# Kernel tuning notes

Measured on AMD Instinct MI355X. Metric: run time of the kernel, lower is better.

Reference implementation:

```python
import jax, jax.numpy as jnp
import numpy as np

N_NODES = 100000

def setup_inputs() -> dict:
    key = jax.random.key(0)
    k1, k2, k3, k4 = jax.random.split(key, 4)
    feat = jax.random.normal(k1, (N_NODES, 128), dtype=jnp.float32)
    weight = jax.random.normal(k2, (128, 64), dtype=jnp.float32) * 0.05
    src = jax.random.randint(k3, (600000,), 0, N_NODES, dtype=jnp.int64)
    dst = jax.random.randint(k4, (600000,), 0, N_NODES, dtype=jnp.int64)
    return {"feat": feat, "weight": weight, "src": src, "dst": dst}

def reference(feat, weight, src, dst):
    n = feat.shape[0]
    ones = jnp.ones(src.shape[0], dtype=jnp.float32)
    # out-degree of source nodes (edges leave src), in-degree of dst nodes
    out_deg = jnp.clip(jax.ops.segment_sum(ones, src, num_segments=n), 1.0)
    in_deg = jnp.clip(jax.ops.segment_sum(ones, dst, num_segments=n), 1.0)
    norm_src = (out_deg ** -0.5)[:, None]   # [N,1]
    norm_dst = (in_deg ** -0.5)[:, None]    # [N,1]
    # in_feats (128) > out_feats (64): project first, then aggregate
    h = jnp.matmul(feat, weight) * norm_src              # [N, 64]
    msgs = h[src]                                        # [E, 64] gather
    rst = jax.ops.segment_sum(msgs, dst, num_segments=n)  # [N, 64] scatter-sum
    rst = rst * norm_dst
    return rst
```

## Files before the change

### kernel.cpp

```cpp
#include <hip/hip_runtime.h>
#include <hip/hip_fp16.h>

#define IN_F 128
#define OUT_F 64
#define NB    256
#define BSH   9
#define CAP   3840
#define CHUNK 2048
#define KPF  136
#define KPW  144

using short8  = __attribute__((ext_vector_type(8))) short;
using float4v = __attribute__((ext_vector_type(4))) float;

static __device__ inline unsigned short f2bf(float x) {
    union { float f; unsigned u; } v; v.f = x;
    unsigned r = (v.u + 0x7fffu + ((v.u >> 16) & 1u)) >> 16;
    return (unsigned short)r;
}

__global__ __launch_bounds__(256) void bin_gemm_kernel(
    const int* __restrict__ src, const int* __restrict__ dst,
    int* __restrict__ gcur_d, int* __restrict__ gcur_s,
    unsigned* __restrict__ bkt_d, unsigned short* __restrict__ bkt_s,
    int E, int nbin,
    const float* __restrict__ feat, const float* __restrict__ W,
    __half* __restrict__ h, int n)
{
    __shared__ union {
        struct { int hd[NB]; int hs[NB]; int based[NB]; int bases[NB]; } bin;
        struct { unsigned short Fh[128 * KPF]; unsigned short Wt[64 * KPW]; } gm;
    } smem;

    const int tid = threadIdx.x;
    const int b   = blockIdx.x;
    const int G   = gridDim.x;
    const int f   = (int)(((long)b       * nbin) / G);
    const int c   = (int)(((long)(b + 1) * nbin) / G);
    const bool is_bin = (c > f);

    if (is_bin) {
        const int e0 = f * CHUNK;

        smem.bin.hd[tid] = 0; smem.bin.hs[tid] = 0;
        __syncthreads();

        int sv[8], dv[8];
        #pragma unroll
        for (int j = 0; j < 8; ++j) {
            int i = e0 + j * 256 + tid;
            if (i < E) { sv[j] = src[i]; dv[j] = dst[i]; }
            else       { sv[j] = -1;     dv[j] = -1; }
        }
        #pragma unroll
        for (int j = 0; j < 8; ++j) {
            if (dv[j] >= 0) {
                atomicAdd(&smem.bin.hd[dv[j] >> BSH], 1);
                atomicAdd(&smem.bin.hs[sv[j] >> BSH], 1);
            }
        }
        __syncthreads();

        int cd = smem.bin.hd[tid], cs = smem.bin.hs[tid];
        smem.bin.based[tid] = cd ? atomicAdd(&gcur_d[tid], cd) : 0;
        smem.bin.bases[tid] = cs ? atomicAdd(&gcur_s[tid], cs) : 0;
        smem.bin.hd[tid] = 0; smem.bin.hs[tid] = 0;
        __syncthreads();

        #pragma unroll
        for (int j = 0; j < 8; ++j) {
            if (dv[j] >= 0) {
                int bd = dv[j] >> BSH;
                int pd = atomicAdd(&smem.bin.hd[bd], 1) + smem.bin.based[bd];
                if (pd < CAP)
                    bkt_d[(size_t)bd * CAP + pd] =
                        (unsigned)sv[j] | ((unsigned)(dv[j] & 511) << 17);
                int bs = sv[j] >> BSH;
                int ps = atomicAdd(&smem.bin.hs[bs], 1) + smem.bin.bases[bs];
                if (ps < CAP) bkt_s[(size_t)bs * CAP + ps] = (unsigned short)(sv[j] & 511);
            }
        }
        return;
    }

    unsigned short* Fh = smem.gm.Fh;
    unsigned short* Wt = smem.gm.Wt;
    const int row0 = (b - f) * 128;

    {
        const float4* W4 = (const float4*)W;
        #pragma unroll
        for (int it = 0; it < 8; ++it) {
            int i4 = it * 256 + tid;
            int k  = i4 >> 4;
            int c4 = (i4 & 15) * 4;
            float4 wv = W4[i4];
            Wt[(c4 + 0) * KPW + k] = f2bf(wv.x);
            Wt[(c4 + 1) * KPW + k] = f2bf(wv.y);
            Wt[(c4 + 2) * KPW + k] = f2bf(wv.z);
            Wt[(c4 + 3) * KPW + k] = f2bf(wv.w);
        }
    }
    {
        const float4* F4 = (const float4*)feat;
        #pragma unroll
        for (int it = 0; it < 16; ++it) {
            int i4 = it * 256 + tid;
            int r  = i4 >> 5;
            int c4 = (i4 & 31) * 4;
            int gr = row0 + r; if (gr >= n) gr = n - 1;
            float4 v = F4[(long)gr * 32 + (i4 & 31)];
            ushort4 u;
            u.x = f2bf(v.x); u.y = f2bf(v.y); u.z = f2bf(v.z); u.w = f2bf(v.w);
            *(ushort4*)&Fh[r * KPF + c4] = u;
        }
    }
    __syncthreads();

    const int w  = tid >> 6;
    const int l  = tid & 63;
    const int ml = l & 15;
    const int q  = l >> 4;

    float4v acc[2][4];
    #pragma unroll
    for (int rt = 0; rt < 2; ++rt)
        #pragma unroll
        for (int ct = 0; ct < 4; ++ct)
            acc[rt][ct] = (float4v){0.f, 0.f, 0.f, 0.f};

    #pragma unroll
    for (int ks = 0; ks < 4; ++ks) {
        const int ko = ks * 32 + q * 8;
        short8 a0 = *(const short8*)&Fh[(w * 32 +  0 + ml) * KPF + ko];
        short8 a1 = *(const short8*)&Fh[(w * 32 + 16 + ml) * KPF + ko];
        short8 b0 = *(const short8*)&Wt[( 0 + ml) * KPW + ko];
        short8 b1 = *(const short8*)&Wt[(16 + ml) * KPW + ko];
        short8 b2 = *(const short8*)&Wt[(32 + ml) * KPW + ko];
        short8 b3 = *(const short8*)&Wt[(48 + ml) * KPW + ko];
        acc[0][0] = __builtin_amdgcn_mfma_f32_16x16x32_bf16(a0, b0, acc[0][0], 0, 0, 0);
        acc[0][1] = __builtin_amdgcn_mfma_f32_16x16x32_bf16(a0, b1, acc[0][1], 0, 0, 0);
        acc[0][2] = __builtin_amdgcn_mfma_f32_16x16x32_bf16(a0, b2, acc[0][2], 0, 0, 0);
        acc[0][3] = __builtin_amdgcn_mfma_f32_16x16x32_bf16(a0, b3, acc[0][3], 0, 0, 0);
        acc[1][0] = __builtin_amdgcn_mfma_f32_16x16x32_bf16(a1, b0, acc[1][0], 0, 0, 0);
        acc[1][1] = __builtin_amdgcn_mfma_f32_16x16x32_bf16(a1, b1, acc[1][1], 0, 0, 0);
        acc[1][2] = __builtin_amdgcn_mfma_f32_16x16x32_bf16(a1, b2, acc[1][2], 0, 0, 0);
        acc[1][3] = __builtin_amdgcn_mfma_f32_16x16x32_bf16(a1, b3, acc[1][3], 0, 0, 0);
    }

    #pragma unroll
    for (int rt = 0; rt < 2; ++rt) {
        #pragma unroll
        for (int reg = 0; reg < 4; ++reg) {
            int row = row0 + w * 32 + rt * 16 + q * 4 + reg;
            if (row < n) {
                #pragma unroll
                for (int ct = 0; ct < 4; ++ct)
                    h[(long)row * OUT_F + ct * 16 + ml] = __float2half(acc[rt][ct][reg]);
            }
        }
    }
}

__global__ __launch_bounds__(256) void csr_kernel(
    const unsigned* __restrict__ bkt_d, const unsigned short* __restrict__ bkt_s,
    const int* __restrict__ gcur_d, const int* __restrict__ gcur_s,
    int2* __restrict__ off_deg, int* __restrict__ ebuf, float* __restrict__ nsrc, int n)
{
    __shared__ int hist[512], curs[512], hist_s[512];
    __shared__ int wsum[4];
    const int b = blockIdx.x, tid = threadIdx.x;
    const int cnt   = min(gcur_d[b], CAP);
    const int cnt_s = min(gcur_s[b], CAP);

    hist[tid] = 0; hist[tid + 256] = 0;
    hist_s[tid] = 0; hist_s[tid + 256] = 0;
    __syncthreads();

    const unsigned* bp = bkt_d + (size_t)b * CAP;
    for (int i = tid; i < cnt; i += 256)
        atomicAdd(&hist[bp[i] >> 17], 1);
    for (int i = tid; i < cnt_s; i += 256)
        atomicAdd(&hist_s[bkt_s[(size_t)b * CAP + i]], 1);
    __syncthreads();

    int a0 = hist[2 * tid], a1 = hist[2 * tid + 1];
    int psum = a0 + a1;
    const int lane = tid & 63, w = tid >> 6;
    int x = psum;
    #pragma unroll
    for (int off = 1; off < 64; off <<= 1) {
        int y = __shfl_up(x, off);
        if (lane >= off) x += y;
    }
    if (lane == 63) wsum[w] = x;
    __syncthreads();
    int wbase = 0;
    for (int i = 0; i < w; ++i) wbase += wsum[i];
    int excl = x + wbase - psum;
    curs[2 * tid]     = excl;
    curs[2 * tid + 1] = excl + a0;
    off_deg[b * 512 + 2 * tid]     = make_int2(b * CAP + excl,      a0);
    off_deg[b * 512 + 2 * tid + 1] = make_int2(b * CAP + excl + a0, a1);
    __syncthreads();

    for (int i = tid; i < cnt; i += 256) {
        unsigned e = bp[i];
        int p = atomicAdd(&curs[e >> 17], 1);
        if (p < CAP) ebuf[b * CAP + p] = (int)(e & 0x1FFFFu);
    }

    int node = b * 512 + tid;
    if (node < n) nsrc[node] = rsqrtf(fmaxf((float)hist_s[tid], 1.0f));
    node += 256;
    if (node < n) nsrc[node] = rsqrtf(fmaxf((float)hist_s[tid + 256], 1.0f));
}

__global__ __launch_bounds__(256) void gather_kernel(
    const int* __restrict__ ebuf, const int2* __restrict__ off_deg,
    const float* __restrict__ nsrc,
    const __half* __restrict__ h, float* __restrict__ out, int n)
{
    const int lane = threadIdx.x & 63;
    const int wv   = threadIdx.x >> 6;
    const int o    = lane >> 3;
    const int t    = lane & 7;
    const int d    = blockIdx.x * 32 + wv * 8 + o;
    if (d >= n) return;

    int2 od = off_deg[d];
    const int beg = od.x, m = od.y, end = beg + m;

    float a0 = 0.f, a1 = 0.f, a2 = 0.f, a3 = 0.f;
    float a4 = 0.f, a5 = 0.f, a6 = 0.f, a7 = 0.f;

    int j = beg;
    for (; j + 1 < end; j += 2) {
        int sA = ebuf[j];
        int sB = ebuf[j + 1];
        float nsA = nsrc[sA];
        float nsB = nsrc[sB];
        union { uint4 u; __half2 h2[4]; } PA, PB;
        PA.u = *(const uint4*)&h[(long)sA * OUT_F + 8 * t];
        PB.u = *(const uint4*)&h[(long)sB * OUT_F + 8 * t];
        float2 fA0 = __half22float2(PA.h2[0]);
        float2 fA1 = __half22float2(PA.h2[1]);
        float2 fA2 = __half22float2(PA.h2[2]);
        float2 fA3 = __half22float2(PA.h2[3]);
        a0 = fmaf(fA0.x, nsA, a0); a1 = fmaf(fA0.y, nsA, a1);
        a2 = fmaf(fA1.x, nsA, a2); a3 = fmaf(fA1.y, nsA, a3);
        a4 = fmaf(fA2.x, nsA, a4); a5 = fmaf(fA2.y, nsA, a5);
        a6 = fmaf(fA3.x, nsA, a6); a7 = fmaf(fA3.y, nsA, a7);
        float2 fB0 = __half22float2(PB.h2[0]);
        float2 fB1 = __half22float2(PB.h2[1]);
        float2 fB2 = __half22float2(PB.h2[2]);
        float2 fB3 = __half22float2(PB.h2[3]);
        a0 = fmaf(fB0.x, nsB, a0); a1 = fmaf(fB0.y, nsB, a1);
        a2 = fmaf(fB1.x, nsB, a2); a3 = fmaf(fB1.y, nsB, a3);
        a4 = fmaf(fB2.x, nsB, a4); a5 = fmaf(fB2.y, nsB, a5);
        a6 = fmaf(fB3.x, nsB, a6); a7 = fmaf(fB3.y, nsB, a7);
    }
    if (j < end) {
        int s = ebuf[j];
        float ns = nsrc[s];
        union { uint4 u; __half2 h2[4]; } P;
        P.u = *(const uint4*)&h[(long)s * OUT_F + 8 * t];
        float2 f0 = __half22float2(P.h2[0]);
        float2 f1 = __half22float2(P.h2[1]);
        float2 f2 = __half22float2(P.h2[2]);
        float2 f3 = __half22float2(P.h2[3]);
        a0 = fmaf(f0.x, ns, a0); a1 = fmaf(f0.y, ns, a1);
        a2 = fmaf(f1.x, ns, a2); a3 = fmaf(f1.y, ns, a3);
        a4 = fmaf(f2.x, ns, a4); a5 = fmaf(f2.y, ns, a5);
        a6 = fmaf(f3.x, ns, a6); a7 = fmaf(f3.y, ns, a7);
    }

    float nd = rsqrtf(fmaxf((float)m, 1.0f));
    float4 v0 = make_float4(a0 * nd, a1 * nd, a2 * nd, a3 * nd);
    float4 v1 = make_float4(a4 * nd, a5 * nd, a6 * nd, a7 * nd);
    float* op = &out[(long)d * OUT_F + 8 * t];
    *(float4*)op       = v0;
    *(float4*)(op + 4) = v1;
}

extern "C" void kernel_launch(void* const* d_in, const int* in_sizes, int n_in,
                              void* d_out, int out_size, void* d_ws, size_t ws_size,
                              hipStream_t stream) {
    const float* feat = (const float*)d_in[0];
    const float* W    = (const float*)d_in[1];
    const int*   src  = (const int*)d_in[2];
    const int*   dst  = (const int*)d_in[3];
    float* out = (float*)d_out;

    const int n = in_sizes[0] / IN_F;
    const int E = in_sizes[2];

    char* wsb = (char*)d_ws;
    int* gcur_d = (int*)wsb;
    int* gcur_s = gcur_d + NB;
    float* nsrc = (float*)(gcur_s + NB);
    size_t pos = (((size_t)(2 * NB + n)) * 4 + 15) & ~(size_t)15;
    int2* off_deg = (int2*)(wsb + pos);
    pos = (pos + (size_t)NB * 512 * 8 + 15) & ~(size_t)15;
    int* ebuf = (int*)(wsb + pos);
    pos = (pos + (size_t)NB * CAP * 4 + 15) & ~(size_t)15;
    unsigned* bkt_d = (unsigned*)(wsb + pos);
    pos = (pos + (size_t)NB * CAP * 4 + 15) & ~(size_t)15;
    unsigned short* bkt_s = (unsigned short*)(wsb + pos);
    pos = (pos + (size_t)NB * CAP * 2 + 15) & ~(size_t)15;
    __half* h = (__half*)(wsb + pos);

    hipMemsetAsync(gcur_d, 0, 2 * NB * sizeof(int), stream);

    const int nbin  = (E + CHUNK - 1) / CHUNK;
    const int ngemm = (n + 127) / 128;

    bin_gemm_kernel<<<nbin + ngemm, 256, 0, stream>>>(src, dst, gcur_d, gcur_s,
                                                      bkt_d, bkt_s, E, nbin,
                                                      feat, W, h, n);
    csr_kernel<<<NB, 256, 0, stream>>>(bkt_d, bkt_s, gcur_d, gcur_s,
                                       off_deg, ebuf, nsrc, n);
    gather_kernel<<<(n + 31) / 32, 256, 0, stream>>>(ebuf, off_deg, nsrc, h, out, n);
}
```

Baseline: 142.8 us.

## Fuse CSR build into gather kernel with atomic task queue and flags

Merges the CSR-building kernel and the gather kernel into one launch. The first 512 dynamically claimed blocks each do a task: either the source-degree histogram for a bucket or the dst bucket counting sort. Every block then spin-waits on a per-bucket ready flag plus a global source-done counter before gathering. This is meant to remove a kernel launch boundary and let gathers on finished buckets overlap with CSR work that is still running. The risks are spin-wait overhead, and the source-norm work is now split into separate tasks that read buckets an extra time.

```diff
diff --git a/kernel.cpp b/kernel.cpp
--- a/kernel.cpp
+++ b/kernel.cpp
@@ -162,65 +162,95 @@
     }
 }
 
-__global__ __launch_bounds__(256) void csr_kernel(
+__global__ __launch_bounds__(256) void csrgather_kernel(
     const unsigned* __restrict__ bkt_d, const unsigned short* __restrict__ bkt_s,
     const int* __restrict__ gcur_d, const int* __restrict__ gcur_s,
-    int2* __restrict__ off_deg, int* __restrict__ ebuf, float* __restrict__ nsrc, int n)
-{
-    __shared__ int hist[512], curs[512], hist_s[512];
-    __shared__ int wsum[4];
-    const int b = blockIdx.x, tid = threadIdx.x;
-    const int cnt   = min(gcur_d[b], CAP);
-    const int cnt_s = min(gcur_s[b], CAP);
-
-    hist[tid] = 0; hist[tid + 256] = 0;
-    hist_s[tid] = 0; hist_s[tid + 256] = 0;
-    __syncthreads();
-
-    const unsigned* bp = bkt_d + (size_t)b * CAP;
-    for (int i = tid; i < cnt; i += 256)
-        atomicAdd(&hist[bp[i] >> 17], 1);
-    for (int i = tid; i < cnt_s; i += 256)
-        atomicAdd(&hist_s[bkt_s[(size_t)b * CAP + i]], 1);
-    __syncthreads();
-
-    int a0 = hist[2 * tid], a1 = hist[2 * tid + 1];
-    int psum = a0 + a1;
-    const int lane = tid & 63, w = tid >> 6;
-    int x = psum;
-    #pragma unroll
-    for (int off = 1; off < 64; off <<= 1) {
-        int y = __shfl_up(x, off);
-        if (lane >= off) x += y;
-    }
-    if (lane == 63) wsum[w] = x;
-    __syncthreads();
-    int wbase = 0;
-    for (int i = 0; i < w; ++i) wbase += wsum[i];
-    int excl = x + wbase - psum;
-    curs[2 * tid]     = excl;
-    curs[2 * tid + 1] = excl + a0;
-    off_deg[b * 512 + 2 * tid]     = make_int2(b * CAP + excl,      a0);
-    off_deg[b * 512 + 2 * tid + 1] = make_int2(b * CAP + excl + a0, a1);
-    __syncthreads();
-
-    for (int i = tid; i < cnt; i += 256) {
-        unsigned e = bp[i];
-        int p = atomicAdd(&curs[e >> 17], 1);
-        if (p < CAP) ebuf[b * CAP + p] = (int)(e & 0x1FFFFu);
-    }
-
-    int node = b * 512 + tid;
-    if (node < n) nsrc[node] = rsqrtf(fmaxf((float)hist_s[tid], 1.0f));
-    node += 256;
-    if (node < n) nsrc[node] = rsqrtf(fmaxf((float)hist_s[tid + 256], 1.0f));
-}
-
-__global__ __launch_bounds__(256) void gather_kernel(
-    const int* __restrict__ ebuf, const int2* __restrict__ off_deg,
-    const float* __restrict__ nsrc,
+    int2* __restrict__ off_deg, int* __restrict__ ebuf, float* __restrict__ nsrc,
+    int* __restrict__ task_cur, int* __restrict__ done_src, int* __restrict__ flags,
     const __half* __restrict__ h, float* __restrict__ out, int n)
 {
+    __shared__ union {
+        struct { int hist[512]; int curs[512]; int wsum[4]; } srt;
+        int hs[512];
+    } sm;
+    __shared__ int s_task;
+
+    const int tid = threadIdx.x;
+
+    if (tid == 0) s_task = atomicAdd(task_cur, 1);
+    __syncthreads();
+    const int task = s_task;
+
+    if (task < 256) {
+        const int b = task;
+        const int cnt_s = min(gcur_s[b], CAP);
+        sm.hs[tid] = 0; sm.hs[tid + 256] = 0;
+        __syncthreads();
+        const unsigned short* sp = bkt_s + (size_t)b * CAP;
+        for (int i = tid; i < cnt_s; i += 256)
+            atomicAdd(&sm.hs[sp[i]], 1);
+        __syncthreads();
+        int node = b * 512 + tid;
+        if (node < n) nsrc[node] = rsqrtf(fmaxf((float)sm.hs[tid], 1.0f));
+        node += 256;
+        if (node < n) nsrc[node] = rsqrtf(fmaxf((float)sm.hs[tid + 256], 1.0f));
+        __syncthreads();
+        if (tid == 0)
+            __hip_atomic_fetch_add(done_src, 1, __ATOMIC_RELEASE,
+                                   __HIP_MEMORY_SCOPE_AGENT);
+    } else if (task < 512) {
+        const int b = task - 256;
+        const int cnt = min(gcur_d[b], CAP);
+        sm.srt.hist[tid] = 0; sm.srt.hist[tid + 256] = 0;
+        __syncthreads();
+        const unsigned* bp = bkt_d + (size_t)b * CAP;
+        for (int i = tid; i < cnt; i += 256)
+            atomicAdd(&sm.srt.hist[bp[i] >> 17], 1);
+        __syncthreads();
+
+        int a0 = sm.srt.hist[2 * tid], a1 = sm.srt.hist[2 * tid + 1];
+        int psum = a0 + a1;
+        const int lane = tid & 63, w = tid >> 6;
+        int x = psum;
+        #pragma unroll
+        for (int off = 1; off < 64; off <<= 1) {
+            int y = __shfl_up(x, off);
+            if (lane >= off) x += y;
+        }
+        if (lane == 63) sm.srt.wsum[w] = x;
+        __syncthreads();
+        int wbase = 0;
+        for (int i = 0; i < w; ++i) wbase += sm.srt.wsum[i];
+        int excl = x + wbase - psum;
+        sm.srt.curs[2 * tid]     = excl;
+        sm.srt.curs[2 * tid + 1] = excl + a0;
+        off_deg[b * 512 + 2 * tid]     = make_int2(b * CAP + excl,      a0);
+        off_deg[b * 512 + 2 * tid + 1] = make_int2(b * CAP + excl + a0, a1);
+        __syncthreads();
+
+        for (int i = tid; i < cnt; i += 256) {
+            unsigned e = bp[i];
+            int p = atomicAdd(&sm.srt.curs[e >> 17], 1);
+            if (p < CAP) ebuf[b * CAP + p] = (int)(e & 0x1FFFFu);
+        }
+        __syncthreads();
+        if (tid == 0)
+            __hip_atomic_store(&flags[b], 1, __ATOMIC_RELEASE,
+                               __HIP_MEMORY_SCOPE_AGENT);
+    }
+
+    const int bkt = blockIdx.x >> 4;
+    if (tid == 0) {
+        while (__hip_atomic_load(done_src, __ATOMIC_RELAXED,
+                                 __HIP_MEMORY_SCOPE_AGENT) < 256 ||
+               __hip_atomic_load(&flags[bkt], __ATOMIC_RELAXED,
+                                 __HIP_MEMORY_SCOPE_AGENT) == 0)
+            __builtin_amdgcn_s_sleep(2);
+    }
+    __syncthreads();
+    (void)__hip_atomic_load(&flags[bkt], __ATOMIC_ACQUIRE,
+                            __HIP_MEMORY_SCOPE_AGENT);
+
     const int lane = threadIdx.x & 63;
     const int wv   = threadIdx.x >> 6;
     const int o    = lane >> 3;
@@ -296,10 +326,13 @@
     const int E = in_sizes[2];
 
     char* wsb = (char*)d_ws;
-    int* gcur_d = (int*)wsb;
-    int* gcur_s = gcur_d + NB;
-    float* nsrc = (float*)(gcur_s + NB);
-    size_t pos = (((size_t)(2 * NB + n)) * 4 + 15) & ~(size_t)15;
+    int* gcur_d   = (int*)wsb;
+    int* gcur_s   = gcur_d + NB;
+    int* task_cur = gcur_s + NB;
+    int* done_src = task_cur + 1;
+    int* flags    = done_src + 1;
+    float* nsrc   = (float*)(flags + NB);
+    size_t pos = (((size_t)(3 * NB + 2 + n)) * 4 + 15) & ~(size_t)15;
     int2* off_deg = (int2*)(wsb + pos);
     pos = (pos + (size_t)NB * 512 * 8 + 15) & ~(size_t)15;
     int* ebuf = (int*)(wsb + pos);
@@ -310,7 +343,7 @@
     pos = (pos + (size_t)NB * CAP * 2 + 15) & ~(size_t)15;
     __half* h = (__half*)(wsb + pos);
 
-    hipMemsetAsync(gcur_d, 0, 2 * NB * sizeof(int), stream);
+    hipMemsetAsync(gcur_d, 0, (3 * NB + 2) * sizeof(int), stream);
 
     const int nbin  = (E + CHUNK - 1) / CHUNK;
     const int ngemm = (n + 127) / 128;
@@ -318,7 +351,8 @@
     bin_gemm_kernel<<<nbin + ngemm, 256, 0, stream>>>(src, dst, gcur_d, gcur_s,
                                                       bkt_d, bkt_s, E, nbin,
                                                       feat, W, h, n);
-    csr_kernel<<<NB, 256, 0, stream>>>(bkt_d, bkt_s, gcur_d, gcur_s,
-                                       off_deg, ebuf, nsrc, n);
-    gather_kernel<<<(n + 31) / 32, 256, 0, stream>>>(ebuf, off_deg, nsrc, h, out, n);
+    csrgather_kernel<<<(n + 31) / 32, 256, 0, stream>>>(bkt_d, bkt_s, gcur_d, gcur_s,
+                                                        off_deg, ebuf, nsrc,
+                                                        task_cur, done_src, flags,
+                                                        h, out, n);
 }
```

Measured after the change: 338.5 us. 2.37x slower.
